# Kernel optimization log

Hardware: AMD Instinct MI355X
Metric: run time of the kernel (lower is better)

Reference implementation:

```python
import jax, jax.numpy as jnp
import numpy as np

DEPTH = 4
HEADS = 8
DIM = 512
MLP = 2048
EPS = 1e-5


def layernorm(x, w, b):
    m = x.mean(-1, keepdims=True)
    v = x.var(-1, keepdims=True)
    return (x - m) * jax.lax.rsqrt(v + EPS) * w + b


def setup_inputs() -> dict:
    key = jax.random.key(0)
    ks = jax.random.split(key, 6)
    s = 0.02
    x = jax.random.normal(ks[0], (4, 2048, DIM), dtype=jnp.float32)
    return {
        "x": x,
        "ln1_w": jnp.ones((DEPTH, DIM), jnp.float32),
        "ln1_b": jnp.zeros((DEPTH, DIM), jnp.float32),
        "qkv_w": jax.random.normal(ks[1], (DEPTH, 3 * DIM, DIM), jnp.float32) * s,
        "proj_w": jax.random.normal(ks[2], (DEPTH, DIM, DIM), jnp.float32) * s,
        "proj_b": jnp.zeros((DEPTH, DIM), jnp.float32),
        "ln2_w": jnp.ones((DEPTH, DIM), jnp.float32),
        "ln2_b": jnp.zeros((DEPTH, DIM), jnp.float32),
        "fc1_w": jax.random.normal(ks[3], (DEPTH, MLP, DIM), jnp.float32) * s,
        "fc1_b": jnp.zeros((DEPTH, MLP), jnp.float32),
        "fc2_w": jax.random.normal(ks[4], (DEPTH, DIM, MLP), jnp.float32) * s,
        "fc2_b": jnp.zeros((DEPTH, DIM), jnp.float32),
    }


def reference(x, ln1_w, ln1_b, qkv_w, proj_w, proj_b, ln2_w, ln2_b, fc1_w, fc1_b, fc2_w, fc2_b):
    B, N, C = x.shape
    Dh = C // HEADS
    scale = Dh ** (-0.5)
    for i in range(DEPTH):
        # PreNorm attention block
        h = layernorm(x, ln1_w[i], ln1_b[i])
        qkv = (h @ qkv_w[i].T).reshape(B, N, 3, HEADS, Dh).transpose(2, 0, 3, 1, 4)
        q, k, v = qkv[0], qkv[1], qkv[2]          # [B,H,N,Dh]
        attn = jax.nn.softmax(jnp.einsum('bhnd,bhmd->bhnm', q, k) * scale, axis=-1)
        o = jnp.einsum('bhnm,bhmd->bhnd', attn, v).transpose(0, 2, 1, 3).reshape(B, N, C)
        x = o @ proj_w[i].T + proj_b[i] + x
        # PreNorm FFN block (exact erf GELU, matching torch nn.GELU default)
        h = layernorm(x, ln2_w[i], ln2_b[i])
        h = jax.nn.gelu(h @ fc1_w[i].T + fc1_b[i], approximate=False)
        x = h @ fc2_w[i].T + fc2_b[i] + x
    return x
```

## Files before the change

kernel.cpp:

```cpp
#include <hip/hip_runtime.h>
#include <hip/hip_bf16.h>
#include <math.h>

#define NB 4
#define HEADS 8
#define DIM 512
#define MLP 2048
#define NT 2048
#define DH 64
#define M_TOK (NB*NT)

typedef __bf16 bf16;
typedef __bf16 bf16x4 __attribute__((ext_vector_type(4)));
typedef __bf16 bf16x8 __attribute__((ext_vector_type(8)));
typedef float f32x4 __attribute__((ext_vector_type(4)));

__device__ __forceinline__ void gl_lds16(const void* g, void* l) {
    __builtin_amdgcn_global_load_lds((const __attribute__((address_space(1))) unsigned int*)g,
                                     (__attribute__((address_space(3))) unsigned int*)l, 16, 0, 0);
}

#define BARRIER() do { __builtin_amdgcn_s_barrier(); asm volatile("" ::: "memory"); } while(0)
#define WAIT_VM4() asm volatile("s_waitcnt vmcnt(4)" ::: "memory")
#define WAIT_VM0() asm volatile("s_waitcnt vmcnt(0)" ::: "memory")

__global__ void cvt_bf16_kernel(const float* __restrict__ src, bf16* __restrict__ dst, int n) {
    int i = (blockIdx.x * 256 + threadIdx.x) * 4;
    if (i < n) {
        float4 v = *(const float4*)(src + i);
        bf16x4 o;
        o[0] = (bf16)v.x; o[1] = (bf16)v.y; o[2] = (bf16)v.z; o[3] = (bf16)v.w;
        *(bf16x4*)(dst + i) = o;
    }
}

__global__ void ln_kernel(const float* __restrict__ X, const float* __restrict__ gam,
                          const float* __restrict__ bet, bf16* __restrict__ out) {
    int w = threadIdx.x >> 6, l = threadIdx.x & 63;
    long row = (long)blockIdx.x * 4 + w;
    const float* xp = X + row * DIM + l * 8;
    float4 a = *(const float4*)xp;
    float4 b = *(const float4*)(xp + 4);
    float s1 = a.x + a.y + a.z + a.w + b.x + b.y + b.z + b.w;
    float s2 = a.x*a.x + a.y*a.y + a.z*a.z + a.w*a.w + b.x*b.x + b.y*b.y + b.z*b.z + b.w*b.w;
#pragma unroll
    for (int off = 32; off; off >>= 1) { s1 += __shfl_xor(s1, off); s2 += __shfl_xor(s2, off); }
    float mean = s1 * (1.f / 512.f);
    float var  = s2 * (1.f / 512.f) - mean * mean;
    float rstd = rsqrtf(var + 1e-5f);
    float4 g0 = *(const float4*)(gam + l * 8), g1 = *(const float4*)(gam + l * 8 + 4);
    float4 b0 = *(const float4*)(bet + l * 8), b1 = *(const float4*)(bet + l * 8 + 4);
    bf16x8 o;
    o[0] = (bf16)((a.x - mean) * rstd * g0.x + b0.x);
    o[1] = (bf16)((a.y - mean) * rstd * g0.y + b0.y);
    o[2] = (bf16)((a.z - mean) * rstd * g0.z + b0.z);
    o[3] = (bf16)((a.w - mean) * rstd * g0.w + b0.w);
    o[4] = (bf16)((b.x - mean) * rstd * g1.x + b1.x);
    o[5] = (bf16)((b.y - mean) * rstd * g1.y + b1.y);
    o[6] = (bf16)((b.z - mean) * rstd * g1.z + b1.z);
    o[7] = (bf16)((b.w - mean) * rstd * g1.w + b1.w);
    *(bf16x8*)(out + row * DIM + l * 8) = o;
}

#define KDIM 512

#define LOADA(AF, B_, MQ) do { \
  _Pragma("unroll") for (int mi_ = 0; mi_ < 4; ++mi_) \
  _Pragma("unroll") for (int kk_ = 0; kk_ < 2; ++kk_) { \
    int row_ = wr * 128 + ((MQ) * 4 + mi_) * 16 + c; \
    AF[mi_][kk_] = *(const bf16x8*)&Abuf[B_][row_ * 64 + (((kk_ * 64 + g * 16) ^ sw) >> 1)]; \
  } } while (0)

#define LOADB(BF, B_, NQ) do { \
  _Pragma("unroll") for (int ni_ = 0; ni_ < 2; ++ni_) \
  _Pragma("unroll") for (int kk_ = 0; kk_ < 2; ++kk_) { \
    int row_ = wc * 64 + ((NQ) * 2 + ni_) * 16 + c; \
    BF[ni_][kk_] = *(const bf16x8*)&Bbuf[B_][row_ * 64 + (((kk_ * 64 + g * 16) ^ sw) >> 1)]; \
  } } while (0)

#define MFMA16(AF, BF, MQ, NQ) do { \
  __builtin_amdgcn_s_setprio(1); \
  _Pragma("unroll") for (int mi_ = 0; mi_ < 4; ++mi_) \
  _Pragma("unroll") for (int ni_ = 0; ni_ < 2; ++ni_) \
  _Pragma("unroll") for (int kk_ = 0; kk_ < 2; ++kk_) \
    acc[(MQ)*4+mi_][(NQ)*2+ni_] = __builtin_amdgcn_mfma_f32_16x16x32_bf16( \
        AF[mi_][kk_], BF[ni_][kk_], acc[(MQ)*4+mi_][(NQ)*2+ni_], 0, 0, 0); \
  __builtin_amdgcn_s_setprio(0); \
} while (0)

#define STAGE_A(J_, MQ) do { int j_ = (J_); if (j_ < nkt) { \
  bf16* db_ = Abuf[j_ & 1]; const bf16* sb_ = Aptr + (size_t)j_ * 64 + coloff; \
  _Pragma("unroll") for (int q_ = 0; q_ < 2; ++q_) { \
    int rpl_ = (MQ) * 64 + q_ * 128 + r0; \
    int rwb_ = (MQ) * 64 + q_ * 128 + (w << 3); \
    gl_lds16(sb_ + (size_t)(arow0 + rpl_) * KDIM, db_ + rwb_ * 64); \
  } } } while (0)

#define STAGE_B(J_, NQ) do { int j_ = (J_); if (j_ < nkt) { \
  bf16* db_ = Bbuf[j_ & 1]; const bf16* sb_ = Wptr + (size_t)j_ * 64 + coloff; \
  _Pragma("unroll") for (int q_ = 0; q_ < 2; ++q_) { \
    int rpl_ = q_ * 128 + ((r0 >> 5) << 6) + (NQ) * 32 + (r0 & 31); \
    int rwb_ = q_ * 128 + (((w << 3) >> 5) << 6) + (NQ) * 32 + ((w << 3) & 31); \
    gl_lds16(sb_ + (size_t)(bcol0 + rpl_) * KDIM, db_ + rwb_ * 64); \
  } } } while (0)

template<int EPI>
__global__ __launch_bounds__(512, 2) void gemm256(const bf16* __restrict__ Aptr,
                                                  const bf16* __restrict__ Wptr,
                                                  const float* __restrict__ bias,
                                                  void* outp, int M, int N) {
    __shared__ bf16 Abuf[2][256 * 64];
    __shared__ bf16 Bbuf[2][256 * 64];
    const int t = threadIdx.x, w = t >> 6, l = t & 63;
    const int wr = w >> 2, wc = w & 3, g = l >> 4, c = l & 15;
    const int sw = (c & 7) << 4;
    const int r0 = (w << 3) + (l >> 3);
    const int coloff = ((l & 7) ^ (l >> 3)) << 3;

    int nwg = gridDim.x;
    int bid = blockIdx.x;
    int q8 = nwg >> 3, r8 = nwg & 7;
    int xcd = bid & 7, rank = bid >> 3;
    int swz = (xcd < r8) ? xcd * (q8 + 1) + rank : r8 * (q8 + 1) + (xcd - r8) * q8 + rank;
    int tiles_n = N >> 8;
    long arow0 = (long)(swz / tiles_n) * 256;
    long bcol0 = (long)(swz % tiles_n) * 256;

    const int nkt = KDIM / 64;
    const int niter = nkt / 2;
    f32x4 acc[8][4] = {};
    bf16x8 af[4][2], bn0[2][2], bn1[2][2];

    STAGE_A(0, 0); STAGE_B(0, 0); STAGE_A(0, 1); STAGE_B(0, 1);
    STAGE_A(1, 0); STAGE_B(1, 0);

#pragma unroll 1
    for (int tt = 0; tt < niter; ++tt) {
        const int J0 = 2 * tt, J1 = 2 * tt + 1;
        const bool last = (tt == niter - 1);
        WAIT_VM4(); BARRIER();
        LOADA(af, 0, 0); LOADB(bn0, 0, 0);
        STAGE_A(J0 + 1, 1);
        MFMA16(af, bn0, 0, 0);
        BARRIER();
        LOADB(bn1, 0, 1);
        STAGE_B(J0 + 1, 1);
        MFMA16(af, bn1, 0, 1);
        BARRIER();
        LOADA(af, 0, 1);
        STAGE_A(J0 + 2, 0);
        MFMA16(af, bn0, 1, 0);
        BARRIER();
        STAGE_B(J0 + 2, 0);
        MFMA16(af, bn1, 1, 1);
        BARRIER();
        if (last) { WAIT_VM0(); } else { WAIT_VM4(); }
        BARRIER();
        LOADA(af, 1, 0); LOADB(bn0, 1, 0);
        STAGE_A(J1 + 1, 1);
        MFMA16(af, bn0, 0, 0);
        BARRIER();
        LOADB(bn1, 1, 1);
        STAGE_B(J1 + 1, 1);
        MFMA16(af, bn1, 0, 1);
        BARRIER();
        LOADA(af, 1, 1);
        STAGE_A(J1 + 2, 0);
        MFMA16(af, bn0, 1, 0);
        BARRIER();
        STAGE_B(J1 + 2, 0);
        MFMA16(af, bn1, 1, 1);
        BARRIER();
    }

#pragma unroll
    for (int m = 0; m < 8; ++m)
#pragma unroll
        for (int n = 0; n < 4; ++n) {
            long row = arow0 + wr * 128 + m * 16 + g * 4;
            long col = bcol0 + wc * 64 + n * 16 + c;
#pragma unroll
            for (int r = 0; r < 4; ++r) {
                float v = acc[m][n][r];
                long rr = row + r;
                if constexpr (EPI == 0) {
                    int o = (int)col;
                    int s = o >> 9, hh = (o >> 6) & 7, d = o & 63;
                    int b = (int)(rr >> 11), nn = (int)(rr & 2047);
                    ((bf16*)outp)[(((long)(s * NB + b) * HEADS + hh) * NT + nn) * DH + d] = (bf16)v;
                } else {
                    float u = v + bias[col];
                    float ge = 0.5f * u * (1.f + erff(u * 0.70710678118654752f));
                    ((bf16*)outp)[rr * N + col] = (bf16)ge;
                }
            }
        }
}

__global__ void gemm_bt(const bf16* __restrict__ A, const bf16* __restrict__ W,
                        const float* __restrict__ bias, const float* resid,
                        float* outp, int M, int N, int K) {
    __shared__ bf16 As[128 * 64];
    __shared__ bf16 Bs[128 * 64];
    int t = threadIdx.x, w = t >> 6, l = t & 63;
    int wr = w >> 1, wc = w & 1, g = l >> 4, c = l & 15;
    long arow0 = (long)blockIdx.y * 128, bcol0 = (long)blockIdx.x * 128;
    f32x4 acc[4][4] = {};
    int lrow = l >> 3, lcol = (l & 7) * 8;
    const bf16* Ab = A + (arow0 + lrow) * (long)K + lcol;
    const bf16* Wb = W + (bcol0 + lrow) * (long)K + lcol;
    for (int k0 = 0; k0 < K; k0 += 64) {
#pragma unroll
        for (int q = 0; q < 4; ++q) {
            int ci = w * 4 + q;
            gl_lds16(Ab + (long)ci * 8 * K + k0, &As[ci * 512]);
            gl_lds16(Wb + (long)ci * 8 * K + k0, &Bs[ci * 512]);
        }
        __syncthreads();
#pragma unroll
        for (int kk = 0; kk < 2; ++kk) {
            bf16x8 afv[4], bfr[4];
#pragma unroll
            for (int m = 0; m < 4; ++m) afv[m] = *(const bf16x8*)&As[(wr * 64 + m * 16 + c) * 64 + kk * 32 + g * 8];
#pragma unroll
            for (int n = 0; n < 4; ++n) bfr[n] = *(const bf16x8*)&Bs[(wc * 64 + n * 16 + c) * 64 + kk * 32 + g * 8];
#pragma unroll
            for (int m = 0; m < 4; ++m)
#pragma unroll
                for (int n = 0; n < 4; ++n)
                    acc[m][n] = __builtin_amdgcn_mfma_f32_16x16x32_bf16(afv[m], bfr[n], acc[m][n], 0, 0, 0);
        }
        __syncthreads();
    }
#pragma unroll
    for (int m = 0; m < 4; ++m)
#pragma unroll
        for (int n = 0; n < 4; ++n) {
            long row = arow0 + wr * 64 + m * 16 + g * 4;
            long col = bcol0 + wc * 64 + n * 16 + c;
#pragma unroll
            for (int r = 0; r < 4; ++r) {
                long rr = row + r;
                outp[rr * N + col] = acc[m][n][r] + bias[col] + resid[rr * N + col];
            }
        }
}

__global__ void attn_kernel(const bf16* __restrict__ qkv, bf16* __restrict__ O) {
    __shared__ bf16 Ks[64 * 64];
    __shared__ bf16 Vt[64 * 64];
    int t = threadIdx.x, w = t >> 6, l = t & 63;
    int g = l >> 4, c = l & 15;
    int qt = blockIdx.x, bh = blockIdx.y;
    long headoff = (long)bh * (NT * DH);
    const bf16* Qb = qkv + headoff;
    const bf16* Kb = qkv + (long)(NB * HEADS) * (NT * DH) + headoff;
    const bf16* Vb = qkv + (long)2 * (NB * HEADS) * (NT * DH) + headoff;
    int q0 = qt * 64 + w * 16;
    bf16x8 qf[2];
    qf[0] = *(const bf16x8*)(Qb + (long)(q0 + c) * DH + g * 8);
    qf[1] = *(const bf16x8*)(Qb + (long)(q0 + c) * DH + 32 + g * 8);
    f32x4 oacc[4] = {};
    float mrun = -__builtin_inff(), lrun = 0.f;
    const float scale = 0.125f;
    int skey = t >> 3, sdh = (t & 7) * 8;
    int vdh = t & 63, vkg = t >> 6;

    for (int kt = 0; kt < NT / 64; ++kt) {
        int key0 = kt * 64;
#pragma unroll
        for (int p = 0; p < 2; ++p) {
            int key = p * 32 + skey;
            bf16x8 kv = *(const bf16x8*)(Kb + (long)(key0 + key) * DH + sdh);
            *(bf16x8*)&Ks[(key * 64 + sdh) ^ ((key & 7) << 3)] = kv;
        }
        {
            const bf16* vp = Vb + (long)(key0 + vkg * 16) * DH + vdh;
            alignas(16) bf16 tmp[16];
#pragma unroll
            for (int i = 0; i < 16; ++i) tmp[i] = vp[(long)i * DH];
            *(bf16x8*)&Vt[(vdh * 64 + vkg * 16) ^ ((vdh & 7) << 3)]     = *(bf16x8*)&tmp[0];
            *(bf16x8*)&Vt[(vdh * 64 + vkg * 16 + 8) ^ ((vdh & 7) << 3)] = *(bf16x8*)&tmp[8];
        }
        __syncthreads();
        f32x4 st[4] = {};
#pragma unroll
        for (int kk = 0; kk < 2; ++kk)
#pragma unroll
            for (int kc = 0; kc < 4; ++kc) {
                int key = kc * 16 + c;
                bf16x8 kf = *(const bf16x8*)&Ks[(key * 64 + kk * 32 + g * 8) ^ ((key & 7) << 3)];
                st[kc] = __builtin_amdgcn_mfma_f32_16x16x32_bf16(kf, qf[kk], st[kc], 0, 0, 0);
            }
        float pv[4][4];
        float mt = -__builtin_inff();
#pragma unroll
        for (int kc = 0; kc < 4; ++kc)
#pragma unroll
            for (int r = 0; r < 4; ++r) { float sv = st[kc][r] * scale; pv[kc][r] = sv; mt = fmaxf(mt, sv); }
        mt = fmaxf(mt, __shfl_xor(mt, 16));
        mt = fmaxf(mt, __shfl_xor(mt, 32));
        float mnew = fmaxf(mrun, mt);
        float fr = __expf(mrun - mnew);
        float ssum = 0.f;
#pragma unroll
        for (int kc = 0; kc < 4; ++kc)
#pragma unroll
            for (int r = 0; r < 4; ++r) { float p = __expf(pv[kc][r] - mnew); pv[kc][r] = p; ssum += p; }
        ssum += __shfl_xor(ssum, 16);
        ssum += __shfl_xor(ssum, 32);
        lrun = lrun * fr + ssum;
        mrun = mnew;
#pragma unroll
        for (int dc = 0; dc < 4; ++dc) oacc[dc] *= fr;
        bf16x8 pf[2];
#pragma unroll
        for (int ks = 0; ks < 2; ++ks)
#pragma unroll
            for (int j = 0; j < 8; ++j) pf[ks][j] = (bf16)pv[2 * ks + (j >> 2)][j & 3];
#pragma unroll
        for (int dc = 0; dc < 4; ++dc) {
            int dh = dc * 16 + c;
            int hwb = dh * 64, swv = (dh & 7) << 3;
#pragma unroll
            for (int ks = 0; ks < 2; ++ks) {
                bf16x4 v0 = *(const bf16x4*)&Vt[(hwb + ks * 32 + g * 4) ^ swv];
                bf16x4 v1 = *(const bf16x4*)&Vt[(hwb + ks * 32 + 16 + g * 4) ^ swv];
                bf16x8 vf = __builtin_shufflevector(v0, v1, 0, 1, 2, 3, 4, 5, 6, 7);
                oacc[dc] = __builtin_amdgcn_mfma_f32_16x16x32_bf16(vf, pf[ks], oacc[dc], 0, 0, 0);
            }
        }
        __syncthreads();
    }
    float inv = 1.f / lrun;
    bf16* ol = &Ks[w * 1024];
#pragma unroll
    for (int dc = 0; dc < 4; ++dc)
#pragma unroll
        for (int r = 0; r < 4; ++r)
            ol[c * 64 + dc * 16 + g * 4 + r] = (bf16)(oacc[dc][r] * inv);
    int qq = l >> 2, dh0 = (l & 3) * 16;
    int b = bh >> 3, hh = bh & 7;
    bf16x8 r0 = *(const bf16x8*)&ol[qq * 64 + dh0];
    bf16x8 r1 = *(const bf16x8*)&ol[qq * 64 + dh0 + 8];
    long tok = (long)b * NT + q0 + qq;
    *(bf16x8*)(O + tok * DIM + hh * 64 + dh0) = r0;
    *(bf16x8*)(O + tok * DIM + hh * 64 + dh0 + 8) = r1;
}

extern "C" void kernel_launch(void* const* d_in, const int* in_sizes, int n_in,
                              void* d_out, int out_size, void* d_ws, size_t ws_size,
                              hipStream_t stream) {
    const float* x      = (const float*)d_in[0];
    const float* ln1_w  = (const float*)d_in[1];
    const float* ln1_b  = (const float*)d_in[2];
    const float* qkv_w  = (const float*)d_in[3];
    const float* proj_w = (const float*)d_in[4];
    const float* proj_b = (const float*)d_in[5];
    const float* ln2_w  = (const float*)d_in[6];
    const float* ln2_b  = (const float*)d_in[7];
    const float* fc1_w  = (const float*)d_in[8];
    const float* fc1_b  = (const float*)d_in[9];
    const float* fc2_w  = (const float*)d_in[10];
    const float* fc2_b  = (const float*)d_in[11];
    float* X = (float*)d_out;

    char* ws = (char*)d_ws;
    bf16* h_bf   = (bf16*)(ws);
    bf16* scr_bf = (bf16*)(ws + (size_t)(8  << 20));
    bf16* o_bf   = (bf16*)(ws + (size_t)(40 << 20));
    bf16* w_qkv  = (bf16*)(ws + (size_t)(48 << 20));
    bf16* w_proj = w_qkv  + (size_t)4 * 1536 * 512;
    bf16* w_fc1  = w_proj + (size_t)4 * 512 * 512;
    bf16* w_fc2  = w_fc1  + (size_t)4 * 2048 * 512;

    {
        int n;
        n = 4 * 1536 * 512; cvt_bf16_kernel<<<n / 1024, 256, 0, stream>>>(qkv_w,  w_qkv,  n);
        n = 4 * 512 * 512;  cvt_bf16_kernel<<<n / 1024, 256, 0, stream>>>(proj_w, w_proj, n);
        n = 4 * 2048 * 512; cvt_bf16_kernel<<<n / 1024, 256, 0, stream>>>(fc1_w,  w_fc1,  n);
        n = 4 * 512 * 2048; cvt_bf16_kernel<<<n / 1024, 256, 0, stream>>>(fc2_w,  w_fc2,  n);
    }
    hipMemcpyAsync(X, x, (size_t)M_TOK * DIM * sizeof(float), hipMemcpyDeviceToDevice, stream);

    for (int i = 0; i < 4; ++i) {
        ln_kernel<<<M_TOK / 4, 256, 0, stream>>>(X, ln1_w + i * 512, ln1_b + i * 512, h_bf);
        gemm256<0><<<(M_TOK / 256) * (1536 / 256), 512, 0, stream>>>(
            h_bf, w_qkv + (size_t)i * 1536 * 512, nullptr, scr_bf, M_TOK, 1536);
        attn_kernel<<<dim3(32, 32), 256, 0, stream>>>(scr_bf, o_bf);
        gemm_bt<<<dim3(4, 64), 256, 0, stream>>>(o_bf, w_proj + (size_t)i * 512 * 512,
                                                 proj_b + i * 512, X, X, M_TOK, 512, 512);
        ln_kernel<<<M_TOK / 4, 256, 0, stream>>>(X, ln2_w + i * 512, ln2_b + i * 512, h_bf);
        gemm256<2><<<(M_TOK / 256) * (2048 / 256), 512, 0, stream>>>(
            h_bf, w_fc1 + (size_t)i * 2048 * 512, fc1_b + i * 2048, scr_bf, M_TOK, 2048);
        gemm_bt<<<dim3(4, 64), 256, 0, stream>>>(scr_bf, w_fc2 + (size_t)i * 512 * 2048,
                                                 fc2_b + i * 512, X, X, M_TOK, 512, 2048);
    }
}
```

Before: 857.8 us.

## Restructure attention with pre-transposed V, async double-buffered K/V loads, 32 queries per wave

Adds a separate kernel that transposes V into a key-contiguous layout. Attention then streams K and V tiles into double-buffered LDS through global_load_lds, issuing the next tile's load while the current one is computed. Each wave now handles 32 queries instead of 16, so each K/V fragment read from LDS feeds more MFMAs. P is staged through LDS with an XOR swizzle to form the PV operands. The cost is an extra kernel launch plus a full write and read of V, and more LDS and register use per block.

```diff
diff --git a/kernel.cpp b/kernel.cpp
--- a/kernel.cpp
+++ b/kernel.cpp
@@ -11,6 +11,7 @@
 #define M_TOK (NB*NT)
 
 typedef __bf16 bf16;
+typedef __bf16 bf16x2 __attribute__((ext_vector_type(2)));
 typedef __bf16 bf16x4 __attribute__((ext_vector_type(4)));
 typedef __bf16 bf16x8 __attribute__((ext_vector_type(8)));
 typedef float f32x4 __attribute__((ext_vector_type(4)));
@@ -246,106 +247,165 @@
         }
 }
 
-__global__ void attn_kernel(const bf16* __restrict__ qkv, bf16* __restrict__ O) {
-    __shared__ bf16 Ks[64 * 64];
-    __shared__ bf16 Vt[64 * 64];
-    int t = threadIdx.x, w = t >> 6, l = t & 63;
-    int g = l >> 4, c = l & 15;
-    int qt = blockIdx.x, bh = blockIdx.y;
-    long headoff = (long)bh * (NT * DH);
-    const bf16* Qb = qkv + headoff;
-    const bf16* Kb = qkv + (long)(NB * HEADS) * (NT * DH) + headoff;
-    const bf16* Vb = qkv + (long)2 * (NB * HEADS) * (NT * DH) + headoff;
-    int q0 = qt * 64 + w * 16;
-    bf16x8 qf[2];
-    qf[0] = *(const bf16x8*)(Qb + (long)(q0 + c) * DH + g * 8);
-    qf[1] = *(const bf16x8*)(Qb + (long)(q0 + c) * DH + 32 + g * 8);
-    f32x4 oacc[4] = {};
-    float mrun = -__builtin_inff(), lrun = 0.f;
-    const float scale = 0.125f;
-    int skey = t >> 3, sdh = (t & 7) * 8;
-    int vdh = t & 63, vkg = t >> 6;
-
+__global__ void vt_kernel(const bf16* __restrict__ qkv, bf16* __restrict__ vt) {
+    __shared__ bf16 tile[64][68];
+    const int t = threadIdx.x;
+    const int kt = blockIdx.x, bh = blockIdx.y;
+    const bf16* V = qkv + (long)2 * (NB * HEADS) * (NT * DH) + (long)bh * (NT * DH) + (long)kt * 64 * DH;
+    bf16* dst = vt + (long)bh * (DH * NT) + kt * 64;
+#pragma unroll
+    for (int i = 0; i < 2; ++i) {
+        int r = i * 32 + (t >> 3);
+        bf16x8 v = *(const bf16x8*)(V + (long)r * DH + (t & 7) * 8);
+        *(bf16x8*)&tile[r][(t & 7) * 8] = v;
+    }
+    __syncthreads();
+#pragma unroll
+    for (int i = 0; i < 2; ++i) {
+        int d = i * 32 + (t >> 3);
+        int k0 = (t & 7) * 8;
+        bf16x8 o;
+#pragma unroll
+        for (int j = 0; j < 8; ++j) o[j] = tile[k0 + j][d];
+        *(bf16x8*)(dst + (long)d * NT + k0) = o;
+    }
+}
+
+#define ATT_STAGE(KT, B_) do { \
+    int key0_ = (KT) * 64; \
+    _Pragma("unroll") for (int i_ = 0; i_ < 2; ++i_) { \
+        int r_ = i_ * 32 + w * 8 + lr; \
+        gl_lds16(Kb + (long)(key0_ + r_) * DH + sch, &Ks[B_][(i_ * 32 + w * 8) * 64]); \
+        gl_lds16(Vtb + (long)r_ * NT + key0_ + sch, &Vs[B_][(i_ * 32 + w * 8) * 64]); \
+    } } while (0)
+
+__global__ __launch_bounds__(256, 2) void attn_kernel(const bf16* __restrict__ qkv,
+                                                      const bf16* __restrict__ vt,
+                                                      bf16* __restrict__ O) {
+    __shared__ bf16 Ks[2][64 * 64];
+    __shared__ bf16 Vs[2][64 * 64];
+    __shared__ bf16 Ps[4][32 * 64];
+    const int t = threadIdx.x, w = t >> 6, l = t & 63;
+    const int g = l >> 4, c = l & 15;
+    const int qt = blockIdx.x, bh = blockIdx.y;
+    const bf16* Qb = qkv + (long)bh * (NT * DH);
+    const bf16* Kb = Qb + (long)(NB * HEADS) * (NT * DH);
+    const bf16* Vtb = vt + (long)bh * (DH * NT);
+    const int q0 = qt * 128 + w * 32;
+    const int lr = l >> 3, lc = l & 7;
+    const int sch = ((lc ^ lr) & 7) * 8;
+    const int xr = (c & 7) << 4;
+
+    bf16x8 qf[2][2];
+#pragma unroll
+    for (int qi = 0; qi < 2; ++qi)
+#pragma unroll
+        for (int kk = 0; kk < 2; ++kk)
+            qf[qi][kk] = *(const bf16x8*)(Qb + (long)(q0 + qi * 16 + c) * DH + kk * 32 + g * 8);
+
+    f32x4 oacc[4][2] = {};
+    float mrun[2] = {-__builtin_inff(), -__builtin_inff()};
+    float lrun[2] = {0.f, 0.f};
+    char* pwave = (char*)&Ps[w][0];
+
+    ATT_STAGE(0, 0);
+#pragma unroll 1
     for (int kt = 0; kt < NT / 64; ++kt) {
-        int key0 = kt * 64;
-#pragma unroll
-        for (int p = 0; p < 2; ++p) {
-            int key = p * 32 + skey;
-            bf16x8 kv = *(const bf16x8*)(Kb + (long)(key0 + key) * DH + sdh);
-            *(bf16x8*)&Ks[(key * 64 + sdh) ^ ((key & 7) << 3)] = kv;
-        }
-        {
-            const bf16* vp = Vb + (long)(key0 + vkg * 16) * DH + vdh;
-            alignas(16) bf16 tmp[16];
-#pragma unroll
-            for (int i = 0; i < 16; ++i) tmp[i] = vp[(long)i * DH];
-            *(bf16x8*)&Vt[(vdh * 64 + vkg * 16) ^ ((vdh & 7) << 3)]     = *(bf16x8*)&tmp[0];
-            *(bf16x8*)&Vt[(vdh * 64 + vkg * 16 + 8) ^ ((vdh & 7) << 3)] = *(bf16x8*)&tmp[8];
-        }
         __syncthreads();
-        f32x4 st[4] = {};
-#pragma unroll
-        for (int kk = 0; kk < 2; ++kk)
-#pragma unroll
-            for (int kc = 0; kc < 4; ++kc) {
-                int key = kc * 16 + c;
-                bf16x8 kf = *(const bf16x8*)&Ks[(key * 64 + kk * 32 + g * 8) ^ ((key & 7) << 3)];
-                st[kc] = __builtin_amdgcn_mfma_f32_16x16x32_bf16(kf, qf[kk], st[kc], 0, 0, 0);
-            }
-        float pv[4][4];
-        float mt = -__builtin_inff();
+        if (kt + 1 < NT / 64) ATT_STAGE(kt + 1, (kt + 1) & 1);
+        const bf16* ksb = &Ks[kt & 1][0];
+        const char* vsb = (const char*)&Vs[kt & 1][0];
+        bf16x8 kf[4][2];
 #pragma unroll
         for (int kc = 0; kc < 4; ++kc)
 #pragma unroll
-            for (int r = 0; r < 4; ++r) { float sv = st[kc][r] * scale; pv[kc][r] = sv; mt = fmaxf(mt, sv); }
-        mt = fmaxf(mt, __shfl_xor(mt, 16));
-        mt = fmaxf(mt, __shfl_xor(mt, 32));
-        float mnew = fmaxf(mrun, mt);
-        float fr = __expf(mrun - mnew);
-        float ssum = 0.f;
+            for (int kk = 0; kk < 2; ++kk)
+                kf[kc][kk] = *(const bf16x8*)&ksb[(kc * 16 + c) * 64 + (((kk * 64 + g * 16) ^ xr) >> 1)];
+        f32x4 st[4][2] = {};
 #pragma unroll
         for (int kc = 0; kc < 4; ++kc)
 #pragma unroll
-            for (int r = 0; r < 4; ++r) { float p = __expf(pv[kc][r] - mnew); pv[kc][r] = p; ssum += p; }
-        ssum += __shfl_xor(ssum, 16);
-        ssum += __shfl_xor(ssum, 32);
-        lrun = lrun * fr + ssum;
-        mrun = mnew;
-#pragma unroll
-        for (int dc = 0; dc < 4; ++dc) oacc[dc] *= fr;
-        bf16x8 pf[2];
+            for (int qi = 0; qi < 2; ++qi)
+#pragma unroll
+                for (int kk = 0; kk < 2; ++kk)
+                    st[kc][qi] = __builtin_amdgcn_mfma_f32_16x16x32_bf16(kf[kc][kk], qf[qi][kk], st[kc][qi], 0, 0, 0);
+#pragma unroll
+        for (int qi = 0; qi < 2; ++qi) {
+            float mt = -__builtin_inff();
+#pragma unroll
+            for (int a = 0; a < 4; ++a)
+#pragma unroll
+                for (int r = 0; r < 4; ++r) mt = fmaxf(mt, st[a][qi][r]);
+            mt = fmaxf(mt, __shfl_xor(mt, 16));
+            mt = fmaxf(mt, __shfl_xor(mt, 32));
+            float mold = mrun[qi];
+            float mnew = fmaxf(mold, mt);
+            float fr = __expf((mold - mnew) * 0.125f);
+            float p[4][4];
+            float ssum = 0.f;
+#pragma unroll
+            for (int a = 0; a < 4; ++a)
+#pragma unroll
+                for (int r = 0; r < 4; ++r) {
+                    float pv = __expf((st[a][qi][r] - mnew) * 0.125f);
+                    p[a][r] = pv; ssum += pv;
+                }
+            ssum += __shfl_xor(ssum, 16);
+            ssum += __shfl_xor(ssum, 32);
+            lrun[qi] = lrun[qi] * fr + ssum;
+            mrun[qi] = mnew;
+#pragma unroll
+            for (int dc = 0; dc < 4; ++dc) oacc[dc][qi] *= fr;
+            int rowb = (qi * 16 + c) * 128;
+#pragma unroll
+            for (int a = 0; a < 4; ++a)
+#pragma unroll
+                for (int rh = 0; rh < 2; ++rh) {
+                    bf16x2 pk; pk[0] = (bf16)p[a][2 * rh]; pk[1] = (bf16)p[a][2 * rh + 1];
+                    *(bf16x2*)(pwave + rowb + ((a * 32 + g * 8 + rh * 4) ^ xr)) = pk;
+                }
+        }
+        bf16x8 pb[2][2], vf[4][2];
 #pragma unroll
         for (int ks = 0; ks < 2; ++ks)
 #pragma unroll
-            for (int j = 0; j < 8; ++j) pf[ks][j] = (bf16)pv[2 * ks + (j >> 2)][j & 3];
-#pragma unroll
-        for (int dc = 0; dc < 4; ++dc) {
-            int dh = dc * 16 + c;
-            int hwb = dh * 64, swv = (dh & 7) << 3;
-#pragma unroll
-            for (int ks = 0; ks < 2; ++ks) {
-                bf16x4 v0 = *(const bf16x4*)&Vt[(hwb + ks * 32 + g * 4) ^ swv];
-                bf16x4 v1 = *(const bf16x4*)&Vt[(hwb + ks * 32 + 16 + g * 4) ^ swv];
-                bf16x8 vf = __builtin_shufflevector(v0, v1, 0, 1, 2, 3, 4, 5, 6, 7);
-                oacc[dc] = __builtin_amdgcn_mfma_f32_16x16x32_bf16(vf, pf[ks], oacc[dc], 0, 0, 0);
-            }
-        }
-        __syncthreads();
-    }
-    float inv = 1.f / lrun;
-    bf16* ol = &Ks[w * 1024];
+            for (int qi = 0; qi < 2; ++qi)
+                pb[ks][qi] = *(const bf16x8*)(pwave + (qi * 16 + c) * 128 + ((ks * 64 + g * 16) ^ xr));
+#pragma unroll
+        for (int dc = 0; dc < 4; ++dc)
+#pragma unroll
+            for (int ks = 0; ks < 2; ++ks)
+                vf[dc][ks] = *(const bf16x8*)(vsb + (dc * 16 + c) * 128 + ((ks * 64 + g * 16) ^ xr));
+#pragma unroll
+        for (int dc = 0; dc < 4; ++dc)
+#pragma unroll
+            for (int ks = 0; ks < 2; ++ks)
+#pragma unroll
+                for (int qi = 0; qi < 2; ++qi)
+                    oacc[dc][qi] = __builtin_amdgcn_mfma_f32_16x16x32_bf16(vf[dc][ks], pb[ks][qi], oacc[dc][qi], 0, 0, 0);
+    }
+    float inv[2] = {1.f / lrun[0], 1.f / lrun[1]};
 #pragma unroll
     for (int dc = 0; dc < 4; ++dc)
 #pragma unroll
-        for (int r = 0; r < 4; ++r)
-            ol[c * 64 + dc * 16 + g * 4 + r] = (bf16)(oacc[dc][r] * inv);
-    int qq = l >> 2, dh0 = (l & 3) * 16;
-    int b = bh >> 3, hh = bh & 7;
-    bf16x8 r0 = *(const bf16x8*)&ol[qq * 64 + dh0];
-    bf16x8 r1 = *(const bf16x8*)&ol[qq * 64 + dh0 + 8];
-    long tok = (long)b * NT + q0 + qq;
-    *(bf16x8*)(O + tok * DIM + hh * 64 + dh0) = r0;
-    *(bf16x8*)(O + tok * DIM + hh * 64 + dh0 + 8) = r1;
+        for (int qi = 0; qi < 2; ++qi) {
+            bf16x4 o4;
+#pragma unroll
+            for (int r = 0; r < 4; ++r) o4[r] = (bf16)(oacc[dc][qi][r] * inv[qi]);
+            *(bf16x4*)(pwave + (qi * 16 + c) * 128 + ((dc * 32 + g * 8) ^ xr)) = o4;
+        }
+    const int orow = l >> 1, ohalf = l & 1;
+    const int bb = bh >> 3, hh = bh & 7;
+    long tok = (long)bb * NT + q0 + orow;
+    bf16* og = (bf16*)O + tok * DIM + hh * 64 + ohalf * 32;
+    const int xr2 = (orow & 7) << 4;
+#pragma unroll
+    for (int j = 0; j < 4; ++j) {
+        bf16x4 v = *(const bf16x4*)(pwave + orow * 128 + ((ohalf * 64 + j * 16) ^ xr2));
+        bf16x4 v2 = *(const bf16x4*)(pwave + orow * 128 + (((ohalf * 64 + j * 16) ^ xr2) + 8));
+        *(bf16x4*)(og + j * 8) = v;
+        *(bf16x4*)(og + j * 8 + 4) = v2;
+    }
 }
 
 extern "C" void kernel_launch(void* const* d_in, const int* in_sizes, int n_in,
@@ -368,6 +428,7 @@
     char* ws = (char*)d_ws;
     bf16* h_bf   = (bf16*)(ws);
     bf16* scr_bf = (bf16*)(ws + (size_t)(8  << 20));
+    bf16* vt_bf  = (bf16*)(ws + (size_t)(32 << 20));
     bf16* o_bf   = (bf16*)(ws + (size_t)(40 << 20));
     bf16* w_qkv  = (bf16*)(ws + (size_t)(48 << 20));
     bf16* w_proj = w_qkv  + (size_t)4 * 1536 * 512;
@@ -387,7 +448,8 @@
         ln_kernel<<<M_TOK / 4, 256, 0, stream>>>(X, ln1_w + i * 512, ln1_b + i * 512, h_bf);
         gemm256<0><<<(M_TOK / 256) * (1536 / 256), 512, 0, stream>>>(
             h_bf, w_qkv + (size_t)i * 1536 * 512, nullptr, scr_bf, M_TOK, 1536);
-        attn_kernel<<<dim3(32, 32), 256, 0, stream>>>(scr_bf, o_bf);
+        vt_kernel<<<dim3(NT / 64, 32), 256, 0, stream>>>(scr_bf, vt_bf);
+        attn_kernel<<<dim3(NT / 128, 32), 256, 0, stream>>>(scr_bf, vt_bf, o_bf);
         gemm_bt<<<dim3(4, 64), 256, 0, stream>>>(o_bf, w_proj + (size_t)i * 512 * 512,
                                                  proj_b + i * 512, X, X, M_TOK, 512, 512);
         ln_kernel<<<M_TOK / 4, 256, 0, stream>>>(X, ln2_w + i * 512, ln2_b + i * 512, h_bf);
```

Measured after the change: 872.2 us. No clear change (+1.7%).
